# Kernel optimization log

Measured on AMD Instinct MI355X. Metric: run time of the kernel, lower is better.

Reference implementation:

```python
import jax, jax.numpy as jnp
import numpy as np

N_NODES = 50000
N_EDGES = 800000
IN_CH = 128
OUT_CH = 64
HID_CH = 2 * OUT_CH  # 128


def gcn_conv(x, edge_index, W, b, n_nodes):
    """PyG GCNConv: linear -> add self-loops -> sym-normalized scatter-add -> bias."""
    h = x @ W  # [N, out]
    loop = jnp.arange(n_nodes)
    row = jnp.concatenate([edge_index[0], loop])  # source nodes
    col = jnp.concatenate([edge_index[1], loop])  # target nodes
    deg = jax.ops.segment_sum(jnp.ones_like(col, dtype=h.dtype), col, num_segments=n_nodes)
    dinv = jnp.where(deg > 0, jax.lax.rsqrt(jnp.maximum(deg, 1.0)), 0.0)
    norm = dinv[row] * dinv[col]  # [E+N]
    msg = h[row] * norm[:, None]  # gather + scale, [E+N, out]
    out = jax.ops.segment_sum(msg, col, num_segments=n_nodes)  # scatter-add
    return out + b


def setup_inputs() -> dict:
    key = jax.random.key(0)
    ks = jax.random.split(key, 9)
    x = jax.random.normal(ks[0], (N_NODES, IN_CH), dtype=jnp.float32)
    edge_index = jax.random.randint(ks[1], (2, N_EDGES), 0, N_NODES, dtype=jnp.int64)
    s_in = 1.0 / np.sqrt(IN_CH)
    s_hid = 1.0 / np.sqrt(HID_CH)
    W1 = jax.random.normal(ks[2], (IN_CH, HID_CH), dtype=jnp.float32) * s_in
    b1 = jnp.zeros((HID_CH,), dtype=jnp.float32)
    W2 = jax.random.normal(ks[3], (HID_CH, OUT_CH), dtype=jnp.float32) * s_hid
    b2 = jnp.zeros((OUT_CH,), dtype=jnp.float32)
    W3 = jax.random.normal(ks[4], (HID_CH, OUT_CH), dtype=jnp.float32) * s_hid
    b3 = jnp.zeros((OUT_CH,), dtype=jnp.float32)
    return {"x": x, "edge_index": edge_index, "W1": W1, "b1": b1,
            "W2": W2, "b2": b2, "W3": W3, "b3": b3}


def reference(x, edge_index, W1, b1, W2, b2, W3, b3):
    act = jax.nn.relu
    hidden = act(gcn_conv(x, edge_index, W1, b1, N_NODES))
    x1 = act(gcn_conv(hidden, edge_index, W2, b2, N_NODES))
    x2 = act(gcn_conv(hidden, edge_index, W3, b3, N_NODES))
    return (x1, x2)
```

## Files before the change

### kernel.cpp

```cpp
#include <hip/hip_runtime.h>

#define N_NODES 50000
#define N_EDGES 800000
#define WT_PAD 136
#define DUMMY N_NODES
#define SLOT_LOG 6
#define AGG_BLKS 3125

#define NB2 782
#define CAP 28
#define EPB 4096
#define PART_BLOCKS 196

typedef __attribute__((ext_vector_type(8))) short short8;
typedef __attribute__((ext_vector_type(4))) float floatx4;

__device__ __forceinline__ short f2bf(float f) {
    union { float f; unsigned u; } v; v.f = f;
    unsigned r = v.u + 0x7fff + ((v.u >> 16) & 1);
    return (short)(r >> 16);
}
__device__ __forceinline__ float bflo(unsigned u) {
    union { unsigned u; float f; } v; v.u = u << 16; return v.f;
}
__device__ __forceinline__ float bfhi(unsigned u) {
    union { unsigned u; float f; } v; v.u = u & 0xffff0000u; return v.f;
}


__global__ __launch_bounds__(256) void partition_prep(const int* __restrict__ ei,
                                                      const float* __restrict__ W1,
                                                      const float* __restrict__ W2,
                                                      const float* __restrict__ W3,
                                                      const float* __restrict__ b2,
                                                      const float* __restrict__ b3,
                                                      unsigned short* __restrict__ Wt1,
                                                      unsigned short* __restrict__ Wt23,
                                                      float* __restrict__ b23,
                                                      int* __restrict__ cnt2d,
                                                      unsigned* __restrict__ bd2,
                                                      unsigned int* __restrict__ gdummy) {
    int tid = threadIdx.x, blk = blockIdx.x;
    if (blk < 66) {
        int i = blk * 256 + tid;
        if (i < 128 * 128) {
            int n = i >> 7, k = i & 127;
            Wt1[i] = (unsigned short)f2bf(W1[k * 128 + n]);
            float w = (n < 64) ? W2[k * 64 + n] : W3[k * 64 + (n - 64)];
            Wt23[i] = (unsigned short)f2bf(w);
        } else if (i < 128 * 128 + 128) {
            int k2 = i - 128 * 128;
            b23[k2] = (k2 < 64) ? b2[k2] : b3[k2 - 64];
        } else if (i < 128 * 128 + 192) {
            gdummy[i - (128 * 128 + 128)] = 0;
        }
    }
    __shared__ int cur[NB2];
    for (int i = tid; i < NB2; i += 256) cur[i] = 0;
    __syncthreads();
    int e0 = blk * EPB;
    int tot = N_EDGES - e0; if (tot > EPB) tot = EPB;
    for (int j = tid; j < tot; j += 256) {
        int e = e0 + j;
        int src = ei[e];
        int d = ei[N_EDGES + e];
        int b = d >> 6;
        int pos = atomicAdd(&cur[b], 1);
        if (pos < CAP)
            bd2[((size_t)blk * NB2 + b) * CAP + pos] = ((unsigned)d << 16) | (unsigned)src;
    }
    __syncthreads();
    for (int b = tid; b < NB2; b += 256) {
        int c = cur[b]; if (c > CAP) c = CAP;
        cnt2d[blk * NB2 + b] = c;
    }
}


template <bool A_BF16>
__global__ __launch_bounds__(256) void csr_gemm(const unsigned* __restrict__ bd2,
                                                const int* __restrict__ cnt2d,
                                                const void* __restrict__ Ain,
                                                const unsigned short* __restrict__ Wt,
                                                int* __restrict__ counts,
                                                unsigned short* __restrict__ sorted_src,
                                                unsigned short* __restrict__ g) {
    __shared__ unsigned short lds[128 * WT_PAD];
    __shared__ int ctr[64];
    int tid = threadIdx.x, b = blockIdx.x;
    uint4* slots4 = (uint4*)lds;
    unsigned short* slots = lds;

    if (tid < 64) ctr[tid] = 0;
    const unsigned dpat = ((unsigned)DUMMY) | (((unsigned)DUMMY) << 16);
    for (int i = tid; i < 512; i += 256) slots4[i] = make_uint4(dpat, dpat, dpat, dpat);
    __syncthreads();

    if (tid < PART_BLOCKS) {
        int cell = tid * NB2 + b;
        int c = cnt2d[cell];
        const unsigned* cp = bd2 + (size_t)cell * CAP;
        for (int j = 0; j < c; ++j) {
            unsigned w = cp[j];
            int dl = (int)((w >> 16) & 63);
            int r = atomicAdd(&ctr[dl], 1);
            if (r < 64) slots[(dl << 6) + r] = (unsigned short)(w & 0xffffu);
        }
    }
    __syncthreads();

    int node0 = b << 6;
    if (tid < 64 && node0 + tid < N_NODES) counts[node0 + tid] = ctr[tid];
    uint4* gs = (uint4*)(sorted_src + ((size_t)node0 << SLOT_LOG));
    for (int k = tid; k < 512; k += 256) {
        int row = k >> 3;
        if (node0 + row < N_NODES) gs[k] = slots4[k];
    }
    __syncthreads();

    int wave = tid >> 6, lane = tid & 63;
    int quad = lane >> 4, ln = lane & 15;
    {
        int r = tid >> 1, h = tid & 1;
        const int4* src = (const int4*)(Wt + r * 128 + h * 64);
#pragma unroll
        for (int i = 0; i < 8; ++i)
            *(int4*)&lds[r * WT_PAD + h * 64 + i * 8] = src[i];
    }
    int row_base = node0 + wave * 16;
    int arow = row_base + ln;
    bool ok = arow < N_NODES;
    short8 afrag[4];
    if (A_BF16) {
        const unsigned short* A = (const unsigned short*)Ain;
#pragma unroll
        for (int kk = 0; kk < 4; ++kk) {
            short8 v = {};
            if (ok) v = *(const short8*)(A + arow * 128 + kk * 32 + quad * 8);
            afrag[kk] = v;
        }
    } else {
        const float* A = (const float*)Ain;
#pragma unroll
        for (int kk = 0; kk < 4; ++kk) {
            short8 v = {};
            if (ok) {
                const floatx4* p = (const floatx4*)(A + arow * 128 + kk * 32 + quad * 8);
                floatx4 fa = p[0], fb = p[1];
                v[0] = f2bf(fa.x); v[1] = f2bf(fa.y); v[2] = f2bf(fa.z); v[3] = f2bf(fa.w);
                v[4] = f2bf(fb.x); v[5] = f2bf(fb.y); v[6] = f2bf(fb.z); v[7] = f2bf(fb.w);
            }
            afrag[kk] = v;
        }
    }
    __syncthreads();

    floatx4 acc[8] = {};
#pragma unroll
    for (int n0 = 0; n0 < 8; ++n0) {
#pragma unroll
        for (int kk = 0; kk < 4; ++kk) {
            short8 bb = *(const short8*)&lds[(n0 * 16 + ln) * WT_PAD + kk * 32 + quad * 8];
            acc[n0] = __builtin_amdgcn_mfma_f32_16x16x32_bf16(afrag[kk], bb, acc[n0], 0, 0, 0);
        }
    }

    __syncthreads();
    unsigned short* st = &lds[wave * 16 * WT_PAD];
    float dv[4];
#pragma unroll
    for (int r = 0; r < 4; ++r) {
        int node = row_base + quad * 4 + r;
        dv[r] = (node < N_NODES) ? rsqrtf((float)(ctr[wave * 16 + quad * 4 + r] + 1)) : 0.f;
    }
#pragma unroll
    for (int n0 = 0; n0 < 8; ++n0)
#pragma unroll
        for (int r = 0; r < 4; ++r)
            st[(quad * 4 + r) * WT_PAD + n0 * 16 + ln] =
                (unsigned short)f2bf(acc[n0][r] * dv[r]);
    __syncthreads();

#pragma unroll
    for (int i = 0; i < 4; ++i) {
        int row = i * 4 + quad;
        int node = row_base + row;
        short8 v = *(const short8*)&st[row * WT_PAD + ln * 8];
        if (node < N_NODES) *(short8*)(g + node * 128 + ln * 8) = v;
    }
}


__global__ __launch_bounds__(256) void gemm_mfma(const unsigned short* __restrict__ A,
                                                 const unsigned short* __restrict__ Wt,
                                                 const int* __restrict__ degs,
                                                 unsigned short* __restrict__ g) {
    __shared__ unsigned short lds[128 * WT_PAD];
    int tid = threadIdx.x;
    int wave = tid >> 6, lane = tid & 63;
    int quad = lane >> 4, ln = lane & 15;

    {
        int r = tid >> 1, h = tid & 1;
        const int4* src = (const int4*)(Wt + r * 128 + h * 64);
#pragma unroll
        for (int i = 0; i < 8; ++i)
            *(int4*)&lds[r * WT_PAD + h * 64 + i * 8] = src[i];
    }

    int row_base = blockIdx.x * 64 + wave * 16;
    int arow = row_base + ln;
    bool ok = arow < N_NODES;
    short8 afrag[4];
#pragma unroll
    for (int kk = 0; kk < 4; ++kk) {
        short8 v = {};
        if (ok) v = *(const short8*)(A + arow * 128 + kk * 32 + quad * 8);
        afrag[kk] = v;
    }
    __syncthreads();

    floatx4 acc[8] = {};
#pragma unroll
    for (int n0 = 0; n0 < 8; ++n0) {
#pragma unroll
        for (int kk = 0; kk < 4; ++kk) {
            short8 b = *(const short8*)&lds[(n0 * 16 + ln) * WT_PAD + kk * 32 + quad * 8];
            acc[n0] = __builtin_amdgcn_mfma_f32_16x16x32_bf16(afrag[kk], b, acc[n0], 0, 0, 0);
        }
    }

    __syncthreads();
    unsigned short* st = &lds[wave * 16 * WT_PAD];
    float dv[4];
#pragma unroll
    for (int r = 0; r < 4; ++r) {
        int node = row_base + quad * 4 + r;
        dv[r] = (node < N_NODES) ? rsqrtf((float)(degs[node] + 1)) : 0.f;
    }
#pragma unroll
    for (int n0 = 0; n0 < 8; ++n0)
#pragma unroll
        for (int r = 0; r < 4; ++r)
            st[(quad * 4 + r) * WT_PAD + n0 * 16 + ln] =
                (unsigned short)f2bf(acc[n0][r] * dv[r]);
    __syncthreads();

#pragma unroll
    for (int i = 0; i < 4; ++i) {
        int row = i * 4 + quad;
        int node = row_base + row;
        short8 v = *(const short8*)&st[row * WT_PAD + ln * 8];
        if (node < N_NODES) *(short8*)(g + node * 128 + ln * 8) = v;
    }
}


template <int MODE>
__global__ __launch_bounds__(256) void aggregate_bf16(const unsigned short* __restrict__ g,
                                                      const int* __restrict__ degs,
                                                      const unsigned short* __restrict__ srcs,
                                                      const float* __restrict__ bias,
                                                      void* __restrict__ outp) {
    int n = blockIdx.x * 16 + (threadIdx.x >> 4);
    int c4 = threadIdx.x & 15;
    const uint4* grow = (const uint4*)g;
    uint4 u = grow[n * 16 + c4];
    float a0 = bflo(u.x), a1 = bfhi(u.x), a2 = bflo(u.y), a3 = bfhi(u.y);
    float a4 = bflo(u.z), a5 = bfhi(u.z), a6 = bflo(u.w), a7 = bfhi(u.w);
    float c0 = 0.f, c1 = 0.f, c2 = 0.f, c3 = 0.f, c5 = 0.f, c6 = 0.f, c7 = 0.f, c8 = 0.f;
    int deg = degs[n];
    int degc = deg > 64 ? 64 : deg;
    int beg = n << SLOT_LOG;
    int pend = beg + ((degc + 3) & ~3);
    int e = beg;
    for (; e + 8 <= pend; e += 8) {
        ushort4 sa = *(const ushort4*)&srcs[e];
        ushort4 sb = *(const ushort4*)&srcs[e + 4];
        uint4 v0 = grow[sa.x * 16 + c4];
        uint4 v1 = grow[sa.y * 16 + c4];
        uint4 v2 = grow[sa.z * 16 + c4];
        uint4 v3 = grow[sa.w * 16 + c4];
        uint4 v4 = grow[sb.x * 16 + c4];
        uint4 v5 = grow[sb.y * 16 + c4];
        uint4 v6 = grow[sb.z * 16 + c4];
        uint4 v7 = grow[sb.w * 16 + c4];
        a0 += bflo(v0.x); a1 += bfhi(v0.x); a2 += bflo(v0.y); a3 += bfhi(v0.y);
        a4 += bflo(v0.z); a5 += bfhi(v0.z); a6 += bflo(v0.w); a7 += bfhi(v0.w);
        c0 += bflo(v1.x); c1 += bfhi(v1.x); c2 += bflo(v1.y); c3 += bfhi(v1.y);
        c5 += bflo(v1.z); c6 += bfhi(v1.z); c7 += bflo(v1.w); c8 += bfhi(v1.w);
        a0 += bflo(v2.x); a1 += bfhi(v2.x); a2 += bflo(v2.y); a3 += bfhi(v2.y);
        a4 += bflo(v2.z); a5 += bfhi(v2.z); a6 += bflo(v2.w); a7 += bfhi(v2.w);
        c0 += bflo(v3.x); c1 += bfhi(v3.x); c2 += bflo(v3.y); c3 += bfhi(v3.y);
        c5 += bflo(v3.z); c6 += bfhi(v3.z); c7 += bflo(v3.w); c8 += bfhi(v3.w);
        a0 += bflo(v4.x); a1 += bfhi(v4.x); a2 += bflo(v4.y); a3 += bfhi(v4.y);
        a4 += bflo(v4.z); a5 += bfhi(v4.z); a6 += bflo(v4.w); a7 += bfhi(v4.w);
        c0 += bflo(v5.x); c1 += bfhi(v5.x); c2 += bflo(v5.y); c3 += bfhi(v5.y);
        c5 += bflo(v5.z); c6 += bfhi(v5.z); c7 += bflo(v5.w); c8 += bfhi(v5.w);
        a0 += bflo(v6.x); a1 += bfhi(v6.x); a2 += bflo(v6.y); a3 += bfhi(v6.y);
        a4 += bflo(v6.z); a5 += bfhi(v6.z); a6 += bflo(v6.w); a7 += bfhi(v6.w);
        c0 += bflo(v7.x); c1 += bfhi(v7.x); c2 += bflo(v7.y); c3 += bfhi(v7.y);
        c5 += bflo(v7.z); c6 += bfhi(v7.z); c7 += bflo(v7.w); c8 += bfhi(v7.w);
    }
    if (e < pend) {
        ushort4 sa = *(const ushort4*)&srcs[e];
        uint4 v0 = grow[sa.x * 16 + c4];
        uint4 v1 = grow[sa.y * 16 + c4];
        uint4 v2 = grow[sa.z * 16 + c4];
        uint4 v3 = grow[sa.w * 16 + c4];
        a0 += bflo(v0.x); a1 += bfhi(v0.x); a2 += bflo(v0.y); a3 += bfhi(v0.y);
        a4 += bflo(v0.z); a5 += bfhi(v0.z); a6 += bflo(v0.w); a7 += bfhi(v0.w);
        c0 += bflo(v1.x); c1 += bfhi(v1.x); c2 += bflo(v1.y); c3 += bfhi(v1.y);
        c5 += bflo(v1.z); c6 += bfhi(v1.z); c7 += bflo(v1.w); c8 += bfhi(v1.w);
        a0 += bflo(v2.x); a1 += bfhi(v2.x); a2 += bflo(v2.y); a3 += bfhi(v2.y);
        a4 += bflo(v2.z); a5 += bfhi(v2.z); a6 += bflo(v2.w); a7 += bfhi(v2.w);
        c0 += bflo(v3.x); c1 += bfhi(v3.x); c2 += bflo(v3.y); c3 += bfhi(v3.y);
        c5 += bflo(v3.z); c6 += bfhi(v3.z); c7 += bflo(v3.w); c8 += bfhi(v3.w);
    }
    a0 += c0; a1 += c1; a2 += c2; a3 += c3; a4 += c5; a5 += c6; a6 += c7; a7 += c8;
    float d = rsqrtf((float)(deg + 1));
    float4 bv0 = ((const float4*)bias)[c4 * 2];
    float4 bv1 = ((const float4*)bias)[c4 * 2 + 1];
    float o0 = fmaxf(d * a0 + bv0.x, 0.f);
    float o1 = fmaxf(d * a1 + bv0.y, 0.f);
    float o2 = fmaxf(d * a2 + bv0.z, 0.f);
    float o3 = fmaxf(d * a3 + bv0.w, 0.f);
    float o4 = fmaxf(d * a4 + bv1.x, 0.f);
    float o5 = fmaxf(d * a5 + bv1.y, 0.f);
    float o6 = fmaxf(d * a6 + bv1.z, 0.f);
    float o7 = fmaxf(d * a7 + bv1.w, 0.f);
    if (MODE == 0) {
        uint4 w;
        w.x = ((unsigned)(unsigned short)f2bf(o0)) | (((unsigned)(unsigned short)f2bf(o1)) << 16);
        w.y = ((unsigned)(unsigned short)f2bf(o2)) | (((unsigned)(unsigned short)f2bf(o3)) << 16);
        w.z = ((unsigned)(unsigned short)f2bf(o4)) | (((unsigned)(unsigned short)f2bf(o5)) << 16);
        w.w = ((unsigned)(unsigned short)f2bf(o6)) | (((unsigned)(unsigned short)f2bf(o7)) << 16);
        ((uint4*)outp)[n * 16 + c4] = w;
    } else {
        int hh = c4 >> 3, cc = c4 & 7;
        float* out = (float*)outp + (size_t)hh * N_NODES * 64;
        floatx4* o = (floatx4*)out + n * 16 + cc * 2;
        floatx4 w0; w0.x = o0; w0.y = o1; w0.z = o2; w0.w = o3;
        floatx4 w1; w1.x = o4; w1.y = o5; w1.z = o6; w1.w = o7;
        __builtin_nontemporal_store(w0, o);
        __builtin_nontemporal_store(w1, o + 1);
    }
}


extern "C" void kernel_launch(void* const* d_in, const int* in_sizes, int n_in,
                              void* d_out, int out_size, void* d_ws, size_t ws_size,
                              hipStream_t stream) {
    const float* x  = (const float*)d_in[0];
    const int*   ei = (const int*)d_in[1];
    const float* W1 = (const float*)d_in[2];
    const float* b1 = (const float*)d_in[3];
    const float* W2 = (const float*)d_in[4];
    const float* b2 = (const float*)d_in[5];
    const float* W3 = (const float*)d_in[6];
    const float* b3 = (const float*)d_in[7];
    float* out = (float*)d_out;

    char* w = (char*)d_ws;
    int*            counts     = (int*)(w + 0);
    int*            cnt2d      = (int*)(w + 200704);
    unsigned short* Wt1        = (unsigned short*)(w + 815104);
    unsigned short* Wt23       = (unsigned short*)(w + 847872);
    float*          b23        = (float*)(w + 880640);
    unsigned short* sorted_src = (unsigned short*)(w + 881152);
    unsigned short* g1         = (unsigned short*)(w + 7281152);
    unsigned*       bd2        = (unsigned*)(w + 20081664);
    unsigned short* hidden     = (unsigned short*)(w + 20081664);

    partition_prep<<<PART_BLOCKS, 256, 0, stream>>>(ei, W1, W2, W3, b2, b3, Wt1, Wt23, b23,
                                                    cnt2d, bd2,
                                                    (unsigned int*)(g1 + N_NODES * 128));

    csr_gemm<false><<<NB2, 256, 0, stream>>>(bd2, cnt2d, x, Wt1, counts, sorted_src, g1);
    aggregate_bf16<0><<<AGG_BLKS, 256, 0, stream>>>(g1, counts, sorted_src, b1, hidden);

    gemm_mfma<<<NB2, 256, 0, stream>>>(hidden, Wt23, counts, g1);
    aggregate_bf16<1><<<AGG_BLKS, 256, 0, stream>>>(g1, counts, sorted_src, b23, out);
}
```

Measured before the change: 190.4 us.

## Split feature matrix into four column planes and aggregate each plane separately

The GEMM kernels now write the bf16 node features as four planes of 32 channels each, and the single aggregation kernel becomes four launches, one per plane. Each plane is about 3.2 MB, so the random neighbour gathers should hit a far smaller working set that fits in L2/LLC. The cost is re-reading the CSR source lists and degrees four times, plus extra launch overhead. Each gather also shrinks to 64 bytes per row instead of 256, which may lower memory efficiency.

```diff
diff --git a/kernel.cpp b/kernel.cpp
--- a/kernel.cpp
+++ b/kernel.cpp
@@ -5,12 +5,13 @@
 #define WT_PAD 136
 #define DUMMY N_NODES
 #define SLOT_LOG 6
-#define AGG_BLKS 3125
+#define PLANE_SH 1600064
 
 #define NB2 782
 #define CAP 28
 #define EPB 4096
 #define PART_BLOCKS 196
+#define AGG_BLKS 782
 
 typedef __attribute__((ext_vector_type(8))) short short8;
 typedef __attribute__((ext_vector_type(4))) float floatx4;
@@ -39,7 +40,7 @@
                                                       float* __restrict__ b23,
                                                       int* __restrict__ cnt2d,
                                                       unsigned* __restrict__ bd2,
-                                                      unsigned int* __restrict__ gdummy) {
+                                                      unsigned short* __restrict__ g1) {
     int tid = threadIdx.x, blk = blockIdx.x;
     if (blk < 66) {
         int i = blk * 256 + tid;
@@ -52,7 +53,9 @@
             int k2 = i - 128 * 128;
             b23[k2] = (k2 < 64) ? b2[k2] : b3[k2 - 64];
         } else if (i < 128 * 128 + 192) {
-            gdummy[i - (128 * 128 + 128)] = 0;
+            int j = i - (128 * 128 + 128);
+            unsigned* p = (unsigned*)(g1 + (size_t)(j >> 4) * PLANE_SH + (size_t)DUMMY * 32);
+            p[j & 15] = 0;
         }
     }
     __shared__ int cur[NB2];
@@ -181,12 +184,14 @@
                 (unsigned short)f2bf(acc[n0][r] * dv[r]);
     __syncthreads();
 
+    int q = ln >> 2, cq = ln & 3;
 #pragma unroll
     for (int i = 0; i < 4; ++i) {
         int row = i * 4 + quad;
         int node = row_base + row;
         short8 v = *(const short8*)&st[row * WT_PAD + ln * 8];
-        if (node < N_NODES) *(short8*)(g + node * 128 + ln * 8) = v;
+        if (node < N_NODES)
+            *(short8*)(g + (size_t)q * PLANE_SH + node * 32 + cq * 8) = v;
     }
 }
 
@@ -246,26 +251,29 @@
                 (unsigned short)f2bf(acc[n0][r] * dv[r]);
     __syncthreads();
 
+    int q = ln >> 2, cq = ln & 3;
 #pragma unroll
     for (int i = 0; i < 4; ++i) {
         int row = i * 4 + quad;
         int node = row_base + row;
         short8 v = *(const short8*)&st[row * WT_PAD + ln * 8];
-        if (node < N_NODES) *(short8*)(g + node * 128 + ln * 8) = v;
+        if (node < N_NODES)
+            *(short8*)(g + (size_t)q * PLANE_SH + node * 32 + cq * 8) = v;
     }
 }
 
 
 template <int MODE>
-__global__ __launch_bounds__(256) void aggregate_bf16(const unsigned short* __restrict__ g,
-                                                      const int* __restrict__ degs,
-                                                      const unsigned short* __restrict__ srcs,
-                                                      const float* __restrict__ bias,
-                                                      void* __restrict__ outp) {
-    int n = blockIdx.x * 16 + (threadIdx.x >> 4);
-    int c4 = threadIdx.x & 15;
-    const uint4* grow = (const uint4*)g;
-    uint4 u = grow[n * 16 + c4];
+__global__ __launch_bounds__(256) void agg_plane(const unsigned short* __restrict__ g,
+                                                 const int* __restrict__ degs,
+                                                 const unsigned short* __restrict__ srcs,
+                                                 const float* __restrict__ bias,
+                                                 void* __restrict__ outp, int plane) {
+    int n = blockIdx.x * 64 + (threadIdx.x >> 2);
+    if (n >= N_NODES) return;
+    int c4 = threadIdx.x & 3;
+    const uint4* grow = (const uint4*)(g + (size_t)plane * PLANE_SH);
+    uint4 u = grow[n * 4 + c4];
     float a0 = bflo(u.x), a1 = bfhi(u.x), a2 = bflo(u.y), a3 = bfhi(u.y);
     float a4 = bflo(u.z), a5 = bfhi(u.z), a6 = bflo(u.w), a7 = bfhi(u.w);
     float c0 = 0.f, c1 = 0.f, c2 = 0.f, c3 = 0.f, c5 = 0.f, c6 = 0.f, c7 = 0.f, c8 = 0.f;
@@ -277,14 +285,14 @@
     for (; e + 8 <= pend; e += 8) {
         ushort4 sa = *(const ushort4*)&srcs[e];
         ushort4 sb = *(const ushort4*)&srcs[e + 4];
-        uint4 v0 = grow[sa.x * 16 + c4];
-        uint4 v1 = grow[sa.y * 16 + c4];
-        uint4 v2 = grow[sa.z * 16 + c4];
-        uint4 v3 = grow[sa.w * 16 + c4];
-        uint4 v4 = grow[sb.x * 16 + c4];
-        uint4 v5 = grow[sb.y * 16 + c4];
-        uint4 v6 = grow[sb.z * 16 + c4];
-        uint4 v7 = grow[sb.w * 16 + c4];
+        uint4 v0 = grow[sa.x * 4 + c4];
+        uint4 v1 = grow[sa.y * 4 + c4];
+        uint4 v2 = grow[sa.z * 4 + c4];
+        uint4 v3 = grow[sa.w * 4 + c4];
+        uint4 v4 = grow[sb.x * 4 + c4];
+        uint4 v5 = grow[sb.y * 4 + c4];
+        uint4 v6 = grow[sb.z * 4 + c4];
+        uint4 v7 = grow[sb.w * 4 + c4];
         a0 += bflo(v0.x); a1 += bfhi(v0.x); a2 += bflo(v0.y); a3 += bfhi(v0.y);
         a4 += bflo(v0.z); a5 += bfhi(v0.z); a6 += bflo(v0.w); a7 += bfhi(v0.w);
         c0 += bflo(v1.x); c1 += bfhi(v1.x); c2 += bflo(v1.y); c3 += bfhi(v1.y);
@@ -304,10 +312,10 @@
     }
     if (e < pend) {
         ushort4 sa = *(const ushort4*)&srcs[e];
-        uint4 v0 = grow[sa.x * 16 + c4];
-        uint4 v1 = grow[sa.y * 16 + c4];
-        uint4 v2 = grow[sa.z * 16 + c4];
-        uint4 v3 = grow[sa.w * 16 + c4];
+        uint4 v0 = grow[sa.x * 4 + c4];
+        uint4 v1 = grow[sa.y * 4 + c4];
+        uint4 v2 = grow[sa.z * 4 + c4];
+        uint4 v3 = grow[sa.w * 4 + c4];
         a0 += bflo(v0.x); a1 += bfhi(v0.x); a2 += bflo(v0.y); a3 += bfhi(v0.y);
         a4 += bflo(v0.z); a5 += bfhi(v0.z); a6 += bflo(v0.w); a7 += bfhi(v0.w);
         c0 += bflo(v1.x); c1 += bfhi(v1.x); c2 += bflo(v1.y); c3 += bfhi(v1.y);
@@ -319,8 +327,8 @@
     }
     a0 += c0; a1 += c1; a2 += c2; a3 += c3; a4 += c5; a5 += c6; a6 += c7; a7 += c8;
     float d = rsqrtf((float)(deg + 1));
-    float4 bv0 = ((const float4*)bias)[c4 * 2];
-    float4 bv1 = ((const float4*)bias)[c4 * 2 + 1];
+    float4 bv0 = ((const float4*)bias)[plane * 8 + c4 * 2];
+    float4 bv1 = ((const float4*)bias)[plane * 8 + c4 * 2 + 1];
     float o0 = fmaxf(d * a0 + bv0.x, 0.f);
     float o1 = fmaxf(d * a1 + bv0.y, 0.f);
     float o2 = fmaxf(d * a2 + bv0.z, 0.f);
@@ -335,15 +343,14 @@
         w.y = ((unsigned)(unsigned short)f2bf(o2)) | (((unsigned)(unsigned short)f2bf(o3)) << 16);
         w.z = ((unsigned)(unsigned short)f2bf(o4)) | (((unsigned)(unsigned short)f2bf(o5)) << 16);
         w.w = ((unsigned)(unsigned short)f2bf(o6)) | (((unsigned)(unsigned short)f2bf(o7)) << 16);
-        ((uint4*)outp)[n * 16 + c4] = w;
+        ((uint4*)outp)[n * 16 + plane * 4 + c4] = w;
     } else {
-        int hh = c4 >> 3, cc = c4 & 7;
-        float* out = (float*)outp + (size_t)hh * N_NODES * 64;
-        floatx4* o = (floatx4*)out + n * 16 + cc * 2;
+        int hh = plane >> 1, cb = (plane & 1) * 32 + c4 * 8;
+        float* out = (float*)outp + (size_t)hh * N_NODES * 64 + (size_t)n * 64 + cb;
         floatx4 w0; w0.x = o0; w0.y = o1; w0.z = o2; w0.w = o3;
         floatx4 w1; w1.x = o4; w1.y = o5; w1.z = o6; w1.w = o7;
-        __builtin_nontemporal_store(w0, o);
-        __builtin_nontemporal_store(w1, o + 1);
+        __builtin_nontemporal_store(w0, (floatx4*)out);
+        __builtin_nontemporal_store(w1, (floatx4*)out + 1);
     }
 }
 
@@ -373,12 +380,13 @@
     unsigned short* hidden     = (unsigned short*)(w + 20081664);
 
     partition_prep<<<PART_BLOCKS, 256, 0, stream>>>(ei, W1, W2, W3, b2, b3, Wt1, Wt23, b23,
-                                                    cnt2d, bd2,
-                                                    (unsigned int*)(g1 + N_NODES * 128));
+                                                    cnt2d, bd2, g1);
 
     csr_gemm<false><<<NB2, 256, 0, stream>>>(bd2, cnt2d, x, Wt1, counts, sorted_src, g1);
-    aggregate_bf16<0><<<AGG_BLKS, 256, 0, stream>>>(g1, counts, sorted_src, b1, hidden);
+    for (int q = 0; q < 4; ++q)
+        agg_plane<0><<<AGG_BLKS, 256, 0, stream>>>(g1, counts, sorted_src, b1, hidden, q);
 
     gemm_mfma<<<NB2, 256, 0, stream>>>(hidden, Wt23, counts, g1);
-    aggregate_bf16<1><<<AGG_BLKS, 256, 0, stream>>>(g1, counts, sorted_src, b23, out);
-}
+    for (int q = 0; q < 4; ++q)
+        agg_plane<1><<<AGG_BLKS, 256, 0, stream>>>(g1, counts, sorted_src, b23, out, q);
+}
```

Measured after the change: 219.8 us. 15.5% more time.
